# Optimization experiments

Measured on AMD Instinct MI355X. Metric: run time of the kernel, lower is better.

## Reference

```python
import jax, jax.numpy as jnp
import numpy as np

P = 2048
D = 1024
H = 16
DH = D // H
HID = 32


def setup_inputs() -> dict:
    key = jax.random.key(0)
    ks = jax.random.split(key, 10)
    s = 0.02
    return {
        "x": jax.random.normal(ks[0], (P, D), jnp.float32),
        "rel": jax.random.normal(ks[1], (P, P, 2), jnp.float32),
        "w_qkv": jax.random.normal(ks[2], (D, 3 * D), jnp.float32) * s,
        "w_proj": jax.random.normal(ks[3], (D, D), jnp.float32) * s,
        "rpb_w1": jax.random.normal(ks[4], (2, HID), jnp.float32) * s,
        "rpb_b1": jnp.zeros((HID,), jnp.float32),
        "rpb_w2": jax.random.normal(ks[5], (HID, HID), jnp.float32) * s,
        "rpb_b2": jnp.zeros((HID,), jnp.float32),
        "rpb_w3": jax.random.normal(ks[6], (HID, 1), jnp.float32) * s,
        "rpb_b3": jnp.zeros((1,), jnp.float32),
    }


def reference(x, rel, w_qkv, w_proj, rpb_w1, rpb_b1, rpb_w2, rpb_b2, rpb_w3, rpb_b3):
    scale = 1.0 / np.sqrt(DH)
    qkv = x @ w_qkv                                   # [P, 3D]
    q, k, v = jnp.split(qkv, 3, axis=-1)
    # [P, D] -> [H, P, DH]
    q = q.reshape(P, H, DH).transpose(1, 0, 2)
    k = k.reshape(P, H, DH).transpose(1, 0, 2)
    v = v.reshape(P, H, DH).transpose(1, 0, 2)
    logits = jnp.einsum('hpd,hqd->hpq', q, k) * scale  # [H, P, P]
    # RelPosBias MLP: (dx,dy) -> scalar, applied over [P, P, 2]
    hcur = jax.nn.relu(rel @ rpb_w1 + rpb_b1)
    hcur = jax.nn.relu(hcur @ rpb_w2 + rpb_b2)
    bias = (hcur @ rpb_w3 + rpb_b3)[..., 0]            # [P, P]
    logits = logits + bias[None]
    attn = jax.nn.softmax(logits, axis=-1)
    out = jnp.einsum('hpq,hqd->hpd', attn, v)          # [H, P, DH]
    out = out.transpose(1, 0, 2).reshape(P, D)
    return out @ w_proj
```

## Files before the change

kernel.cpp:

```cpp
#include <hip/hip_runtime.h>
#include <hip/hip_bf16.h>
#include <type_traits>

typedef __attribute__((ext_vector_type(8))) short bf16x8;
typedef __attribute__((ext_vector_type(4))) float floatx4;
typedef __attribute__((ext_vector_type(2))) float float2v;

__device__ __forceinline__ float bf2f(unsigned short u) {
    union { unsigned int x; float f; } v; v.x = ((unsigned int)u) << 16; return v.f;
}
__device__ __forceinline__ unsigned short f2bf(float f) {
    union { float f; unsigned int u; } v; v.f = f;
    unsigned int x = v.u;
    unsigned int r = x + 0x7fffu + ((x >> 16) & 1u);
    return (unsigned short)(r >> 16);
}

typedef const __attribute__((address_space(1))) unsigned int u32_g;
typedef __attribute__((address_space(3))) unsigned int u32_l;
__device__ __forceinline__ void gld_lds16(const void* g, void* l) {
    __builtin_amdgcn_global_load_lds((u32_g*)g, (u32_l*)l, 16, 0, 0);
}

__device__ __forceinline__ void trans32(const float* __restrict__ in,
                                        unsigned short* __restrict__ out,
                                        int K, int N, int bx, int by,
                                        unsigned short (*T)[33]) {
    const int n0 = bx * 32, k0 = by * 32;
    const int r = threadIdx.x >> 3;
    const int c4 = (threadIdx.x & 7) * 4;
    float4 v = *reinterpret_cast<const float4*>(in + (size_t)(k0 + r) * N + n0 + c4);
    T[c4 + 0][r] = f2bf(v.x);
    T[c4 + 1][r] = f2bf(v.y);
    T[c4 + 2][r] = f2bf(v.z);
    T[c4 + 3][r] = f2bf(v.w);
    __syncthreads();
    ushort4 o = {T[r][c4], T[r][c4 + 1], T[r][c4 + 2], T[r][c4 + 3]};
    *reinterpret_cast<ushort4*>(out + (size_t)(n0 + r) * K + k0 + c4) = o;
}

__global__ __launch_bounds__(256) void prep(const float* __restrict__ x,
                                            unsigned short* __restrict__ xb,
                                            const float* __restrict__ wq,
                                            unsigned short* __restrict__ wqT,
                                            const float* __restrict__ wp,
                                            unsigned short* __restrict__ wpT) {
    __shared__ unsigned short T[32][33];
    const int b = blockIdx.x;
    if (b < 1024) {
        size_t i = ((size_t)b * 256 + threadIdx.x) * 8;
        float4 a = *reinterpret_cast<const float4*>(x + i);
        float4 c = *reinterpret_cast<const float4*>(x + i + 4);
        unsigned short t[8] = {f2bf(a.x), f2bf(a.y), f2bf(a.z), f2bf(a.w),
                               f2bf(c.x), f2bf(c.y), f2bf(c.z), f2bf(c.w)};
        *reinterpret_cast<uint4*>(xb + i) = *reinterpret_cast<const uint4*>(t);
    } else if (b < 4096) {
        int t = b - 1024;
        trans32(wq, wqT, 1024, 3072, t % 96, t / 96, T);
    } else {
        int t = b - 4096;
        trans32(wp, wpT, 1024, 1024, t % 32, t / 32, T);
    }
}

template<int BN, typename TC>
__global__ __launch_bounds__(256) void gemm_abt(const unsigned short* __restrict__ A,
                                                const unsigned short* __restrict__ Bt,
                                                TC* __restrict__ C,
                                                int M, int N, int K) {
    constexpr int NT = BN / 32;
    __shared__ __align__(16) unsigned short As[64 * 32];
    __shared__ __align__(16) unsigned short Bs[BN * 32];

    const int tid = threadIdx.x;
    const int wave = tid >> 6;
    const int lane = tid & 63;
    const int m15 = lane & 15;
    const int quad = lane >> 4;
    const int wm = wave >> 1;
    const int wn = wave & 1;
    const int m0 = blockIdx.y * 64;
    const int n0 = blockIdx.x * BN;

    const int srow = lane >> 2;
    const int scol = (lane & 3) * 8;

    floatx4 acc[2][NT];
#pragma unroll
    for (int mt = 0; mt < 2; mt++)
#pragma unroll
        for (int nt = 0; nt < NT; nt++) acc[mt][nt] = {0.f, 0.f, 0.f, 0.f};

    for (int k0 = 0; k0 < K; k0 += 32) {
        gld_lds16(A + (size_t)(m0 + wave * 16 + srow) * K + k0 + scol, &As[wave * 16 * 32]);
#pragma unroll
        for (int i = 0; i < BN / 64; i++) {
            int j = wave * (BN / 64) + i;
            gld_lds16(Bt + (size_t)(n0 + j * 16 + srow) * K + k0 + scol, &Bs[j * 16 * 32]);
        }
        __syncthreads();

        bf16x8 a[2];
#pragma unroll
        for (int mt = 0; mt < 2; mt++)
            a[mt] = *reinterpret_cast<bf16x8*>(&As[(wm * 32 + mt * 16 + m15) * 32 + quad * 8]);
#pragma unroll
        for (int nt = 0; nt < NT; nt++) {
            bf16x8 b = *reinterpret_cast<bf16x8*>(&Bs[(wn * (BN / 2) + nt * 16 + m15) * 32 + quad * 8]);
#pragma unroll
            for (int mt = 0; mt < 2; mt++)
                acc[mt][nt] = __builtin_amdgcn_mfma_f32_16x16x32_bf16(a[mt], b, acc[mt][nt], 0, 0, 0);
        }
        __syncthreads();
    }

#pragma unroll
    for (int mt = 0; mt < 2; mt++)
#pragma unroll
        for (int nt = 0; nt < NT; nt++)
#pragma unroll
            for (int i = 0; i < 4; i++) {
                int row = m0 + wm * 32 + mt * 16 + quad * 4 + i;
                int col = n0 + wn * (BN / 2) + nt * 16 + m15;
                if constexpr (std::is_same<TC, float>::value)
                    C[(size_t)row * N + col] = acc[mt][nt][i];
                else
                    C[(size_t)row * N + col] = f2bf(acc[mt][nt][i]);
            }
}

__global__ __launch_bounds__(256) void rpb_mfma_kernel(const float* __restrict__ rel,
                                                       const float* __restrict__ w1,
                                                       const float* __restrict__ b1,
                                                       const float* __restrict__ w2,
                                                       const float* __restrict__ b2,
                                                       const float* __restrict__ w3,
                                                       const float* __restrict__ b3,
                                                       unsigned short* __restrict__ biasb) {
    __shared__ __align__(16) unsigned short Ah[4][64 * 40];

    const int tid = threadIdx.x;
    const int wave = tid >> 6;
    const int lane = tid & 63;
    const int m15 = lane & 15;
    const int quad = lane >> 4;

    float2v w1a2[16], w1b2[16], b12[16];
#pragma unroll
    for (int cp = 0; cp < 16; cp++) {
        w1a2[cp] = {w1[2 * cp], w1[2 * cp + 1]};
        w1b2[cp] = {w1[32 + 2 * cp], w1[32 + 2 * cp + 1]};
        b12[cp]  = {b1[2 * cp], b1[2 * cp + 1]};
    }

    bf16x8 bf0, bf1;
    {
        unsigned short t0[8], t1[8];
#pragma unroll
        for (int j = 0; j < 8; j++) {
            int k = quad * 8 + j;
            t0[j] = f2bf(w2[k * 32 + m15]);
            t1[j] = f2bf(w2[k * 32 + 16 + m15]);
        }
        bf0 = *reinterpret_cast<bf16x8*>(t0);
        bf1 = *reinterpret_cast<bf16x8*>(t1);
    }
    const float b2a = b2[m15], b2b = b2[16 + m15];
    const float2v w3a2 = {w3[m15], w3[m15]};
    const float2v w3b2 = {w3[16 + m15], w3[16 + m15]};
    const float b3v = b3[0];
    const float LOG2E = 1.44269504f;
    const float2v z2 = {0.f, 0.f};

    unsigned short* myA = Ah[wave];
    const int base = blockIdx.x * 1024 + wave * 64;

    for (int it = 0; it < 4; ++it) {
        const int pix0 = base + it * 256;
        float2 dxy = *reinterpret_cast<const float2*>(rel + (size_t)(pix0 + lane) * 2);
        float2v dx2 = {dxy.x, dxy.x}, dy2 = {dxy.y, dxy.y};

        unsigned int hp[16];
#pragma unroll
        for (int cp = 0; cp < 16; cp++) {
            float2v h = __builtin_elementwise_fma(dx2, w1a2[cp],
                         __builtin_elementwise_fma(dy2, w1b2[cp], b12[cp]));
            h = __builtin_elementwise_max(h, z2);
            hp[cp] = __builtin_amdgcn_perm(__float_as_uint(h.y), __float_as_uint(h.x), 0x07060302u);
        }
#pragma unroll
        for (int ch = 0; ch < 4; ch++)
            *reinterpret_cast<uint4*>(&myA[lane * 40 + ch * 8]) = *reinterpret_cast<const uint4*>(&hp[ch * 4]);

#pragma unroll
        for (int t = 0; t < 4; t++) {
            bf16x8 a = *reinterpret_cast<bf16x8*>(&myA[(t * 16 + m15) * 40 + quad * 8]);
            floatx4 d0 = {b2a, b2a, b2a, b2a};
            floatx4 d1 = {b2b, b2b, b2b, b2b};
            d0 = __builtin_amdgcn_mfma_f32_16x16x32_bf16(a, bf0, d0, 0, 0, 0);
            d1 = __builtin_amdgcn_mfma_f32_16x16x32_bf16(a, bf1, d1, 0, 0, 0);

            float2v p0 = __builtin_elementwise_max(__builtin_shufflevector(d0, d0, 0, 1), z2);
            float2v p1 = __builtin_elementwise_max(__builtin_shufflevector(d0, d0, 2, 3), z2);
            float2v q0 = __builtin_elementwise_max(__builtin_shufflevector(d1, d1, 0, 1), z2);
            float2v q1 = __builtin_elementwise_max(__builtin_shufflevector(d1, d1, 2, 3), z2);
            float2v s01 = __builtin_elementwise_fma(q0, w3b2, p0 * w3a2);
            float2v s23 = __builtin_elementwise_fma(q1, w3b2, p1 * w3a2);
            float s[4] = {s01.x, s01.y, s23.x, s23.y};

#pragma unroll
            for (int i = 0; i < 4; i++) {
                int iv;
                iv = __builtin_amdgcn_update_dpp(__float_as_int(s[i]), __float_as_int(s[i]), 0x121, 0xf, 0xf, false);
                s[i] += __int_as_float(iv);
                iv = __builtin_amdgcn_update_dpp(__float_as_int(s[i]), __float_as_int(s[i]), 0x122, 0xf, 0xf, false);
                s[i] += __int_as_float(iv);
                iv = __builtin_amdgcn_update_dpp(__float_as_int(s[i]), __float_as_int(s[i]), 0x124, 0xf, 0xf, false);
                s[i] += __int_as_float(iv);
                iv = __builtin_amdgcn_update_dpp(__float_as_int(s[i]), __float_as_int(s[i]), 0x128, 0xf, 0xf, false);
                s[i] += __int_as_float(iv);
            }
            if (m15 == 0) {
                unsigned short o[4];
#pragma unroll
                for (int i = 0; i < 4; i++) o[i] = f2bf((s[i] + b3v) * LOG2E);
                *reinterpret_cast<ushort4*>(biasb + (size_t)pix0 + t * 16 + quad * 4) =
                    *reinterpret_cast<const ushort4*>(o);
            }
        }
    }
}

__global__ __launch_bounds__(256) void attn_kernel(const unsigned short* __restrict__ qkv,
                                                   const unsigned short* __restrict__ biasb,
                                                   unsigned short* __restrict__ attn_out) {
    const int h = blockIdx.x;
    const int q0 = blockIdx.y * 64;
    __shared__ __align__(16) unsigned short Qs[64 * 72];
    __shared__ __align__(16) unsigned short Ks[2][64 * 72];
    __shared__ __align__(16) unsigned short Vst[2][64 * 72];
    __shared__ __align__(16) unsigned short Ps[4][16 * 72];

    const int tid = threadIdx.x;
    const int wave = tid >> 6;
    const int lane = tid & 63;
    const int m15 = lane & 15;
    const int quad = lane >> 4;

    for (int c = tid; c < 512; c += 256) {
        int r = c >> 3, d0 = (c & 7) * 8;
        *reinterpret_cast<float4*>(&Qs[r * 72 + d0]) =
            *reinterpret_cast<const float4*>(qkv + (size_t)(q0 + r) * 3072 + h * 64 + d0);
    }

    const int kr0 = tid >> 3, kd0 = (tid & 7) * 8;
    const int vkey = tid & 63;
    const int vd0 = (tid >> 6) * 8;

    uint4 kreg0 = *reinterpret_cast<const uint4*>(qkv + (size_t)kr0 * 3072 + 1024 + h * 64 + kd0);
    uint4 kreg1 = *reinterpret_cast<const uint4*>(qkv + (size_t)(kr0 + 32) * 3072 + 1024 + h * 64 + kd0);
    uint4 vreg0 = *reinterpret_cast<const uint4*>(qkv + (size_t)vkey * 3072 + 2048 + h * 64 + vd0);
    uint4 vreg1 = *reinterpret_cast<const uint4*>(qkv + (size_t)vkey * 3072 + 2048 + h * 64 + vd0 + 32);
    unsigned short br[16];
#pragma unroll
    for (int nt = 0; nt < 4; nt++)
#pragma unroll
        for (int i = 0; i < 4; i++)
            br[nt * 4 + i] = biasb[(size_t)(q0 + wave * 16 + quad * 4 + i) * 2048 + nt * 16 + m15];

    float rs[4] = {0.f, 0.f, 0.f, 0.f};
    floatx4 acc[4];
#pragma unroll
    for (int i = 0; i < 4; i++) acc[i] = {0.f, 0.f, 0.f, 0.f};
    const float c1 = 0.125f * 1.44269504f;

    for (int kt = 0; kt < 32; ++kt) {
        unsigned short* Kc = Ks[kt & 1];
        unsigned short* Vc = Vst[kt & 1];

        *reinterpret_cast<uint4*>(&Kc[kr0 * 72 + kd0]) = kreg0;
        *reinterpret_cast<uint4*>(&Kc[(kr0 + 32) * 72 + kd0]) = kreg1;
        {
            const unsigned short* t = reinterpret_cast<const unsigned short*>(&vreg0);
#pragma unroll
            for (int j = 0; j < 8; j++) Vc[(vd0 + j) * 72 + vkey] = t[j];
        }
        {
            const unsigned short* t = reinterpret_cast<const unsigned short*>(&vreg1);
#pragma unroll
            for (int j = 0; j < 8; j++) Vc[(vd0 + 32 + j) * 72 + vkey] = t[j];
        }
        __syncthreads();

        if (kt < 31) {
            const size_t kb = (size_t)(kt + 1) * 64;
            kreg0 = *reinterpret_cast<const uint4*>(qkv + (kb + kr0) * 3072 + 1024 + h * 64 + kd0);
            kreg1 = *reinterpret_cast<const uint4*>(qkv + (kb + kr0 + 32) * 3072 + 1024 + h * 64 + kd0);
            vreg0 = *reinterpret_cast<const uint4*>(qkv + (kb + vkey) * 3072 + 2048 + h * 64 + vd0);
            vreg1 = *reinterpret_cast<const uint4*>(qkv + (kb + vkey) * 3072 + 2048 + h * 64 + vd0 + 32);
        }

        floatx4 s[4];
#pragma unroll
        for (int nt = 0; nt < 4; nt++) s[nt] = {0.f, 0.f, 0.f, 0.f};
#pragma unroll
        for (int kh = 0; kh < 2; kh++) {
            bf16x8 a = *reinterpret_cast<bf16x8*>(&Qs[(wave * 16 + m15) * 72 + kh * 32 + quad * 8]);
#pragma unroll
            for (int nt = 0; nt < 4; nt++) {
                bf16x8 b = *reinterpret_cast<bf16x8*>(&Kc[(nt * 16 + m15) * 72 + kh * 32 + quad * 8]);
                s[nt] = __builtin_amdgcn_mfma_f32_16x16x32_bf16(a, b, s[nt], 0, 0, 0);
            }
        }

        float p[4][4];
#pragma unroll
        for (int nt = 0; nt < 4; nt++)
#pragma unroll
            for (int i = 0; i < 4; i++) {
                float lg = fmaf(s[nt][i], c1, bf2f(br[nt * 4 + i]));
                p[nt][i] = __builtin_amdgcn_exp2f(lg);
                rs[i] += p[nt][i];
            }

        if (kt < 31) {
            const int kb = (kt + 1) * 64;
#pragma unroll
            for (int nt = 0; nt < 4; nt++)
#pragma unroll
                for (int i = 0; i < 4; i++)
                    br[nt * 4 + i] = biasb[(size_t)(q0 + wave * 16 + quad * 4 + i) * 2048 + kb + nt * 16 + m15];
        }

        unsigned short* Pw = Ps[wave];
#pragma unroll
        for (int nt = 0; nt < 4; nt++)
#pragma unroll
            for (int i = 0; i < 4; i++)
                Pw[(quad * 4 + i) * 72 + nt * 16 + m15] = f2bf(p[nt][i]);
        __asm__ volatile("s_waitcnt lgkmcnt(0)" ::: "memory");

#pragma unroll
        for (int kh = 0; kh < 2; kh++) {
            bf16x8 a = *reinterpret_cast<bf16x8*>(&Pw[m15 * 72 + kh * 32 + quad * 8]);
#pragma unroll
            for (int nt = 0; nt < 4; nt++) {
                bf16x8 b = *reinterpret_cast<bf16x8*>(&Vc[(nt * 16 + m15) * 72 + kh * 32 + quad * 8]);
                acc[nt] = __builtin_amdgcn_mfma_f32_16x16x32_bf16(a, b, acc[nt], 0, 0, 0);
            }
        }
    }

    float linv[4];
#pragma unroll
    for (int i = 0; i < 4; i++) {
        float r = rs[i];
        r += __shfl_xor(r, 1);
        r += __shfl_xor(r, 2);
        r += __shfl_xor(r, 4);
        r += __shfl_xor(r, 8);
        linv[i] = 1.f / r;
    }
#pragma unroll
    for (int nt = 0; nt < 4; nt++)
#pragma unroll
        for (int i = 0; i < 4; i++) {
            int row = q0 + wave * 16 + quad * 4 + i;
            int col = h * 64 + nt * 16 + m15;
            attn_out[(size_t)row * 1024 + col] = f2bf(acc[nt][i] * linv[i]);
        }
}

extern "C" void kernel_launch(void* const* d_in, const int* in_sizes, int n_in,
                              void* d_out, int out_size, void* d_ws, size_t ws_size,
                              hipStream_t stream) {
    const float* x      = (const float*)d_in[0];
    const float* rel    = (const float*)d_in[1];
    const float* w_qkv  = (const float*)d_in[2];
    const float* w_proj = (const float*)d_in[3];
    const float* w1     = (const float*)d_in[4];
    const float* b1     = (const float*)d_in[5];
    const float* w2     = (const float*)d_in[6];
    const float* b2     = (const float*)d_in[7];
    const float* w3     = (const float*)d_in[8];
    const float* b3     = (const float*)d_in[9];

    char* ws = (char*)d_ws;
    unsigned short* qkv   = (unsigned short*)ws;
    unsigned short* biasb = (unsigned short*)(ws + 12582912);
    unsigned short* xb    = (unsigned short*)(ws + 20971520);
    unsigned short* attn  = xb;
    unsigned short* wqT   = (unsigned short*)(ws + 25165824);
    unsigned short* wpT   = (unsigned short*)(ws + 31457280);
    float* out = (float*)d_out;

    prep<<<5120, 256, 0, stream>>>(x, xb, w_qkv, wqT, w_proj, wpT);
    gemm_abt<128, unsigned short><<<dim3(24, 32), 256, 0, stream>>>(xb, wqT, qkv, 2048, 3072, 1024);
    rpb_mfma_kernel<<<4096, 256, 0, stream>>>(rel, w1, b1, w2, b2, w3, b3, biasb);
    attn_kernel<<<dim3(16, 32), 256, 0, stream>>>(qkv, biasb, attn);
    gemm_abt<64, float><<<dim3(16, 32), 256, 0, stream>>>(attn, wpT, out, 2048, 1024, 1024);
}
```

Measured before the change: 247.5 us.

## Split attention key range across two wave groups per block and merge partials

The attention kernel now launches 512 threads per block as two groups of four waves. Each group handles half of the 2048 keys with its own K/V shared buffers, and the two partial accumulators and row sums are combined through shared memory at the end. Q fragments are kept in registers instead of shared memory, and the V transpose writes packed 32-bit pairs using byte permutes rather than scalar 16-bit stores. The aim is more waves in flight and fewer serial iterations per block. The cost is an extra reduction stage, an added barrier per iteration, and more register pressure from the launch bounds.

```diff
diff --git a/kernel.cpp b/kernel.cpp
--- a/kernel.cpp
+++ b/kernel.cpp
@@ -231,42 +231,47 @@
     }
 }
 
-__global__ __launch_bounds__(256) void attn_kernel(const unsigned short* __restrict__ qkv,
-                                                   const unsigned short* __restrict__ biasb,
-                                                   unsigned short* __restrict__ attn_out) {
+__global__ __launch_bounds__(512, 4) void attn_kernel(const unsigned short* __restrict__ qkv,
+                                                      const unsigned short* __restrict__ biasb,
+                                                      unsigned short* __restrict__ attn_out) {
     const int h = blockIdx.x;
     const int q0 = blockIdx.y * 64;
-    __shared__ __align__(16) unsigned short Qs[64 * 72];
-    __shared__ __align__(16) unsigned short Ks[2][64 * 72];
+    __shared__ __align__(16) unsigned short Kst[2][64 * 72];
     __shared__ __align__(16) unsigned short Vst[2][64 * 72];
-    __shared__ __align__(16) unsigned short Ps[4][16 * 72];
+    __shared__ __align__(16) unsigned short Ps[8][16 * 72];
 
     const int tid = threadIdx.x;
-    const int wave = tid >> 6;
+    const int g = tid >> 8;
+    const int w = (tid >> 6) & 3;
     const int lane = tid & 63;
+    const int ltid = tid & 255;
     const int m15 = lane & 15;
     const int quad = lane >> 4;
 
-    for (int c = tid; c < 512; c += 256) {
-        int r = c >> 3, d0 = (c & 7) * 8;
-        *reinterpret_cast<float4*>(&Qs[r * 72 + d0]) =
-            *reinterpret_cast<const float4*>(qkv + (size_t)(q0 + r) * 3072 + h * 64 + d0);
-    }
-
-    const int kr0 = tid >> 3, kd0 = (tid & 7) * 8;
-    const int vkey = tid & 63;
-    const int vd0 = (tid >> 6) * 8;
-
-    uint4 kreg0 = *reinterpret_cast<const uint4*>(qkv + (size_t)kr0 * 3072 + 1024 + h * 64 + kd0);
-    uint4 kreg1 = *reinterpret_cast<const uint4*>(qkv + (size_t)(kr0 + 32) * 3072 + 1024 + h * 64 + kd0);
-    uint4 vreg0 = *reinterpret_cast<const uint4*>(qkv + (size_t)vkey * 3072 + 2048 + h * 64 + vd0);
-    uint4 vreg1 = *reinterpret_cast<const uint4*>(qkv + (size_t)vkey * 3072 + 2048 + h * 64 + vd0 + 32);
+    bf16x8 qf[2];
+#pragma unroll
+    for (int kh = 0; kh < 2; kh++)
+        qf[kh] = *reinterpret_cast<const bf16x8*>(
+            qkv + (size_t)(q0 + w * 16 + m15) * 3072 + h * 64 + kh * 32 + quad * 8);
+
+    const int kr0 = ltid >> 3, kd0 = (ltid & 7) * 8;
+    const int ka = (ltid & 31) * 2;
+    const int vd0 = (ltid >> 5) * 8;
+
+    unsigned short* Kc = Kst[g];
+    unsigned short* Vc = Vst[g];
+    const size_t kofs = (size_t)g * 1024;
+
+    uint4 kreg0 = *reinterpret_cast<const uint4*>(qkv + (kofs + kr0) * 3072 + 1024 + h * 64 + kd0);
+    uint4 kreg1 = *reinterpret_cast<const uint4*>(qkv + (kofs + kr0 + 32) * 3072 + 1024 + h * 64 + kd0);
+    uint4 vrega = *reinterpret_cast<const uint4*>(qkv + (kofs + ka) * 3072 + 2048 + h * 64 + vd0);
+    uint4 vregb = *reinterpret_cast<const uint4*>(qkv + (kofs + ka + 1) * 3072 + 2048 + h * 64 + vd0);
     unsigned short br[16];
 #pragma unroll
     for (int nt = 0; nt < 4; nt++)
 #pragma unroll
         for (int i = 0; i < 4; i++)
-            br[nt * 4 + i] = biasb[(size_t)(q0 + wave * 16 + quad * 4 + i) * 2048 + nt * 16 + m15];
+            br[nt * 4 + i] = biasb[(size_t)(q0 + w * 16 + quad * 4 + i) * 2048 + kofs + nt * 16 + m15];
 
     float rs[4] = {0.f, 0.f, 0.f, 0.f};
     floatx4 acc[4];
@@ -274,30 +279,30 @@
     for (int i = 0; i < 4; i++) acc[i] = {0.f, 0.f, 0.f, 0.f};
     const float c1 = 0.125f * 1.44269504f;
 
-    for (int kt = 0; kt < 32; ++kt) {
-        unsigned short* Kc = Ks[kt & 1];
-        unsigned short* Vc = Vst[kt & 1];
+    for (int kt = 0; kt < 16; ++kt) {
+        __syncthreads();
 
         *reinterpret_cast<uint4*>(&Kc[kr0 * 72 + kd0]) = kreg0;
         *reinterpret_cast<uint4*>(&Kc[(kr0 + 32) * 72 + kd0]) = kreg1;
         {
-            const unsigned short* t = reinterpret_cast<const unsigned short*>(&vreg0);
-#pragma unroll
-            for (int j = 0; j < 8; j++) Vc[(vd0 + j) * 72 + vkey] = t[j];
-        }
-        {
-            const unsigned short* t = reinterpret_cast<const unsigned short*>(&vreg1);
-#pragma unroll
-            for (int j = 0; j < 8; j++) Vc[(vd0 + 32 + j) * 72 + vkey] = t[j];
+            const unsigned int* aw = reinterpret_cast<const unsigned int*>(&vrega);
+            const unsigned int* bw = reinterpret_cast<const unsigned int*>(&vregb);
+#pragma unroll
+            for (int wd = 0; wd < 4; wd++) {
+                unsigned int lo = __builtin_amdgcn_perm(bw[wd], aw[wd], 0x05040100u);
+                unsigned int hi = __builtin_amdgcn_perm(bw[wd], aw[wd], 0x07060302u);
+                *reinterpret_cast<unsigned int*>(&Vc[(vd0 + 2 * wd) * 72 + ka]) = lo;
+                *reinterpret_cast<unsigned int*>(&Vc[(vd0 + 2 * wd + 1) * 72 + ka]) = hi;
+            }
         }
         __syncthreads();
 
-        if (kt < 31) {
-            const size_t kb = (size_t)(kt + 1) * 64;
+        if (kt < 15) {
+            const size_t kb = kofs + (size_t)(kt + 1) * 64;
             kreg0 = *reinterpret_cast<const uint4*>(qkv + (kb + kr0) * 3072 + 1024 + h * 64 + kd0);
             kreg1 = *reinterpret_cast<const uint4*>(qkv + (kb + kr0 + 32) * 3072 + 1024 + h * 64 + kd0);
-            vreg0 = *reinterpret_cast<const uint4*>(qkv + (kb + vkey) * 3072 + 2048 + h * 64 + vd0);
-            vreg1 = *reinterpret_cast<const uint4*>(qkv + (kb + vkey) * 3072 + 2048 + h * 64 + vd0 + 32);
+            vrega = *reinterpret_cast<const uint4*>(qkv + (kb + ka) * 3072 + 2048 + h * 64 + vd0);
+            vregb = *reinterpret_cast<const uint4*>(qkv + (kb + ka + 1) * 3072 + 2048 + h * 64 + vd0);
         }
 
         floatx4 s[4];
@@ -305,11 +310,10 @@
         for (int nt = 0; nt < 4; nt++) s[nt] = {0.f, 0.f, 0.f, 0.f};
 #pragma unroll
         for (int kh = 0; kh < 2; kh++) {
-            bf16x8 a = *reinterpret_cast<bf16x8*>(&Qs[(wave * 16 + m15) * 72 + kh * 32 + quad * 8]);
 #pragma unroll
             for (int nt = 0; nt < 4; nt++) {
                 bf16x8 b = *reinterpret_cast<bf16x8*>(&Kc[(nt * 16 + m15) * 72 + kh * 32 + quad * 8]);
-                s[nt] = __builtin_amdgcn_mfma_f32_16x16x32_bf16(a, b, s[nt], 0, 0, 0);
+                s[nt] = __builtin_amdgcn_mfma_f32_16x16x32_bf16(qf[kh], b, s[nt], 0, 0, 0);
             }
         }
 
@@ -323,16 +327,16 @@
                 rs[i] += p[nt][i];
             }
 
-        if (kt < 31) {
-            const int kb = (kt + 1) * 64;
+        if (kt < 15) {
+            const size_t kb = kofs + (size_t)(kt + 1) * 64;
 #pragma unroll
             for (int nt = 0; nt < 4; nt++)
 #pragma unroll
                 for (int i = 0; i < 4; i++)
-                    br[nt * 4 + i] = biasb[(size_t)(q0 + wave * 16 + quad * 4 + i) * 2048 + kb + nt * 16 + m15];
-        }
-
-        unsigned short* Pw = Ps[wave];
+                    br[nt * 4 + i] = biasb[(size_t)(q0 + w * 16 + quad * 4 + i) * 2048 + kb + nt * 16 + m15];
+        }
+
+        unsigned short* Pw = Ps[tid >> 6];
 #pragma unroll
         for (int nt = 0; nt < 4; nt++)
 #pragma unroll
@@ -351,7 +355,7 @@
         }
     }
 
-    float linv[4];
+    float rsum[4];
 #pragma unroll
     for (int i = 0; i < 4; i++) {
         float r = rs[i];
@@ -359,16 +363,40 @@
         r += __shfl_xor(r, 2);
         r += __shfl_xor(r, 4);
         r += __shfl_xor(r, 8);
-        linv[i] = 1.f / r;
-    }
-#pragma unroll
-    for (int nt = 0; nt < 4; nt++)
-#pragma unroll
-        for (int i = 0; i < 4; i++) {
-            int row = q0 + wave * 16 + quad * 4 + i;
-            int col = h * 64 + nt * 16 + m15;
-            attn_out[(size_t)row * 1024 + col] = f2bf(acc[nt][i] * linv[i]);
-        }
+        rsum[i] = r;
+    }
+
+    float* accbuf = reinterpret_cast<float*>(&Kst[0][0]);
+    float* lbuf = accbuf + 4096;
+
+    __syncthreads();
+    if (g == 1) {
+#pragma unroll
+        for (int nt = 0; nt < 4; nt++)
+#pragma unroll
+            for (int i = 0; i < 4; i++)
+                accbuf[(w * 16 + quad * 4 + i) * 64 + nt * 16 + m15] = acc[nt][i];
+        if (m15 == 0) {
+#pragma unroll
+            for (int i = 0; i < 4; i++) lbuf[w * 16 + quad * 4 + i] = rsum[i];
+        }
+    }
+    __syncthreads();
+    if (g == 0) {
+        float linv[4];
+#pragma unroll
+        for (int i = 0; i < 4; i++)
+            linv[i] = 1.f / (rsum[i] + lbuf[w * 16 + quad * 4 + i]);
+#pragma unroll
+        for (int nt = 0; nt < 4; nt++)
+#pragma unroll
+            for (int i = 0; i < 4; i++) {
+                float o = (acc[nt][i] + accbuf[(w * 16 + quad * 4 + i) * 64 + nt * 16 + m15]) * linv[i];
+                int row = q0 + w * 16 + quad * 4 + i;
+                int col = h * 64 + nt * 16 + m15;
+                attn_out[(size_t)row * 1024 + col] = f2bf(o);
+            }
+    }
 }
 
 extern "C" void kernel_launch(void* const* d_in, const int* in_sizes, int n_in,
@@ -397,6 +425,6 @@
     prep<<<5120, 256, 0, stream>>>(x, xb, w_qkv, wqT, w_proj, wpT);
     gemm_abt<128, unsigned short><<<dim3(24, 32), 256, 0, stream>>>(xb, wqT, qkv, 2048, 3072, 1024);
     rpb_mfma_kernel<<<4096, 256, 0, stream>>>(rel, w1, b1, w2, b2, w3, b3, biasb);
-    attn_kernel<<<dim3(16, 32), 256, 0, stream>>>(qkv, biasb, attn);
+    attn_kernel<<<dim3(16, 32), 512, 0, stream>>>(qkv, biasb, attn);
     gemm_abt<64, float><<<dim3(16, 32), 256, 0, stream>>>(attn, wpT, out, 2048, 1024, 1024);
 }
```

After: 233.6 us. -5.6%, faster.
